# Kernel tuning notes

Hardware: AMD Instinct MI355X
Metric: run time of the kernel (lower is better)

Reference implementation:

```python
import jax, jax.numpy as jnp
import numpy as np

B, L = 64, 512
D_IN, D_POS = 256, 64
KS, VS, H = 64, 64, 8
OUT = 256
EPS = 1e-5
NEG = -1e30


def setup_inputs() -> dict:
    key = jax.random.key(0)
    ks = jax.random.split(key, 12)
    D = D_IN + D_POS
    s = 0.02
    return {
        "emb": jax.random.normal(ks[0], (B, L, D_IN), jnp.float32),
        "boxes": jax.random.normal(ks[1], (B, L, D_POS), jnp.float32),
        "lengths": jax.random.randint(ks[2], (B,), 1, L + 1, jnp.int32),
        "Wq": jax.random.normal(ks[3], (D, H * KS), jnp.float32) * s,
        "Wk": jax.random.normal(ks[4], (D, H * KS), jnp.float32) * s,
        "Wv": jax.random.normal(ks[5], (D, H * VS), jnp.float32) * s,
        "W1": jax.random.normal(ks[6], (H * VS, OUT), jnp.float32) * s,
        "b1": jnp.zeros((OUT,), jnp.float32),
        "W2": jax.random.normal(ks[7], (OUT, OUT), jnp.float32) * s,
        "b2": jnp.zeros((OUT,), jnp.float32),
        "g1": jnp.ones((OUT,), jnp.float32),
        "be1": jnp.zeros((OUT,), jnp.float32),
        "g2": jnp.ones((OUT,), jnp.float32),
        "be2": jnp.zeros((OUT,), jnp.float32),
    }


def masked_bn(x, m, cnt, gamma, beta):
    # BatchNorm1d (training stats) over valid tokens only; x: [B,L,C], m: [B,L,1]
    mean = jnp.sum(x * m, axis=(0, 1)) / cnt
    var = jnp.sum(((x - mean) ** 2) * m, axis=(0, 1)) / cnt
    return gamma * (x - mean) * jax.lax.rsqrt(var + EPS) + beta


def reference(emb, boxes, lengths, Wq, Wk, Wv, W1, b1, W2, b2, g1, be1, g2, be2):
    X = jnp.concatenate([emb, boxes], axis=-1)  # [B,L,D]
    valid = (jnp.arange(L)[None, :] < lengths[:, None])  # [B,L] bool
    m = valid[..., None].astype(X.dtype)  # [B,L,1]
    cnt = jnp.sum(m)

    D = X.shape[-1]
    Q = jnp.einsum('bld,dhk->bhlk', X, Wq.reshape(D, H, KS))
    K = jnp.einsum('bld,dhk->bhlk', X, Wk.reshape(D, H, KS))
    V = jnp.einsum('bld,dhv->bhlv', X, Wv.reshape(D, H, VS))

    scores = jnp.einsum('bhqk,bhmk->bhqm', Q, K) / jnp.sqrt(jnp.float32(KS))
    scores = jnp.where(valid[:, None, None, :], scores, NEG)  # mask keys
    A = jax.nn.softmax(scores, axis=-1)  # [B,H,L,L]
    Z = jnp.einsum('bhqm,bhmv->bhqv', A, V)  # [B,H,L,V]
    Z = jnp.transpose(Z, (0, 2, 1, 3)).reshape(B, L, H * VS)

    # agregate: Linear -> BN -> ReLU -> (dropout=identity, eval) -> Linear -> BN + skip -> ReLU
    Z1 = Z @ W1 + b1
    Z1 = jax.nn.relu(masked_bn(Z1, m, cnt, g1, be1)) * m
    Z2 = Z1 @ W2 + b2
    out = jax.nn.relu(masked_bn(Z2, m, cnt, g2, be2) + emb) * m
    return out  # padded [B,L,OUT]; invalid positions zeroed
```

## Files before the change

kernel.cpp:

```cpp
#include <hip/hip_runtime.h>
#include <hip/hip_bf16.h>
#include <cstdio>

#define B_    64
#define L_    512
#define DIN   256
#define DPOS  64
#define DD    320
#define HH    8
#define ROWS  (B_*L_)
#define NQKV  1536

typedef __attribute__((ext_vector_type(4))) float floatx4;
typedef __attribute__((ext_vector_type(8))) __bf16 bf16x8;
typedef __attribute__((ext_vector_type(4))) __bf16 bf16x4;

static __device__ __forceinline__ floatx4 mfma_bf16(bf16x8 a, bf16x8 b, floatx4 c) {
  return __builtin_amdgcn_mfma_f32_16x16x32_bf16(a, b, c, 0, 0, 0);
}

#define GLOAD_LDS(gp, lp) \
  __builtin_amdgcn_global_load_lds((const __attribute__((address_space(1))) void*)(gp), \
                                   (__attribute__((address_space(3))) void*)(lp), 16, 0, 0)

__global__ __launch_bounds__(256)
void prep_emb(const float* __restrict__ emb, __hip_bfloat16* __restrict__ X) {
  int idx = blockIdx.x * 256 + threadIdx.x;
  int row = idx >> 6, c4 = (idx & 63) * 4;
  const float4 v = *(const float4*)(emb + (size_t)idx * 4);
  bf16x4 o; o[0] = (__bf16)v.x; o[1] = (__bf16)v.y; o[2] = (__bf16)v.z; o[3] = (__bf16)v.w;
  *(bf16x4*)((__bf16*)X + (size_t)row * DD + c4) = o;
}

__global__ __launch_bounds__(256)
void prep_box(const float* __restrict__ boxes, __hip_bfloat16* __restrict__ X) {
  int idx = blockIdx.x * 256 + threadIdx.x;
  int row = idx >> 4, c4 = (idx & 15) * 4;
  const float4 v = *(const float4*)(boxes + (size_t)idx * 4);
  bf16x4 o; o[0] = (__bf16)v.x; o[1] = (__bf16)v.y; o[2] = (__bf16)v.z; o[3] = (__bf16)v.w;
  *(bf16x4*)((__bf16*)X + (size_t)row * DD + DIN + c4) = o;
}

__global__ __launch_bounds__(256)
void prep_w(const float* __restrict__ Wq, const float* __restrict__ Wk,
            const float* __restrict__ Wv, const float* __restrict__ W1,
            const float* __restrict__ W2,
            __hip_bfloat16* __restrict__ WqkvT, __hip_bfloat16* __restrict__ W1T,
            __hip_bfloat16* __restrict__ W2T) {
  int n = blockIdx.x, t = threadIdx.x;
  if (n < NQKV) {
    const float* W = (n < 512) ? Wq : (n < 1024) ? Wk : Wv;
    int nn = n & 511;
    for (int k = t; k < DD; k += 256)
      WqkvT[(size_t)n*DD + k] = __float2bfloat16(W[(size_t)k*512 + nn]);
  } else if (n < NQKV + 256) {
    int nn = n - NQKV;
    for (int k = t; k < 512; k += 256)
      W1T[(size_t)nn*512 + k] = __float2bfloat16(W1[(size_t)k*256 + nn]);
  } else {
    int nn = n - NQKV - 256;
    for (int k = t; k < 256; k += 256)
      W2T[(size_t)nn*256 + k] = __float2bfloat16(W2[(size_t)k*256 + nn]);
  }
}

template<int EPI>
__global__ __launch_bounds__(256, 4)
void gemm_bt(const __hip_bfloat16* __restrict__ A, const __hip_bfloat16* __restrict__ BT,
             int nbx, int M, int N, int K, int lda,
             float* __restrict__ outF, const float* __restrict__ bias,
             __hip_bfloat16* __restrict__ outQK, __hip_bfloat16* __restrict__ outVT,
             const int* __restrict__ lengths, float* __restrict__ pS,
             float* __restrict__ pS2) {
  __shared__ __align__(16) __bf16 sm[17408];
  int hw = blockIdx.x;
  int lidx = (hw & 7) * ((int)gridDim.x >> 3) + (hw >> 3);
  int bx = lidx % nbx, by = lidx / nbx;
  int t = threadIdx.x;
  int m0 = by * 128, n0 = bx * 128;
  int wave = t >> 6, lane = t & 63, lr = lane & 15, lg = lane >> 4;
  int wr = wave >> 1, wc = wave & 1;
  floatx4 acc[4][4];
#pragma unroll
  for (int i = 0; i < 4; ++i)
#pragma unroll
    for (int j = 0; j < 4; ++j)
#pragma unroll
      for (int q = 0; q < 4; ++q) acc[i][j][q] = 0.f;

  int srow = t >> 2, ssl = t & 3;
  int scb = ssl ^ ((srow >> 2) & 3);
  const __bf16* gA = (const __bf16*)A + (size_t)(m0 + srow) * lda + scb * 8;
  const __bf16* gB = (const __bf16*)BT + (size_t)(n0 + srow) * K + scb * 8;

  auto stage = [&](int k0, int buf) {
    __bf16* Ad = sm + buf * 4096;
    __bf16* Bd = sm + 8192 + buf * 4096;
    GLOAD_LDS(gA + k0, Ad + t * 8);
    GLOAD_LDS(gA + (size_t)64 * lda + k0, Ad + (256 + t) * 8);
    GLOAD_LDS(gB + k0, Bd + t * 8);
    GLOAD_LDS(gB + (size_t)64 * K + k0, Bd + (256 + t) * 8);
  };

  int fs = (lr >> 2) & 3;
  int aoff[4], boff[4];
#pragma unroll
  for (int i = 0; i < 4; ++i) {
    aoff[i] = (wr*64 + i*16 + lr) * 32 + ((lg ^ fs) * 8);
    boff[i] = (wc*64 + i*16 + lr) * 32 + ((lg ^ fs) * 8);
  }

  int NK = K >> 5;
  stage(0, 0);
  __syncthreads();
  for (int kt = 0; kt < NK; ++kt) {
    int cur = kt & 1;
    if (kt + 1 < NK) stage((kt + 1) << 5, cur ^ 1);
    const __bf16* As = sm + cur * 4096;
    const __bf16* Bs = sm + 8192 + cur * 4096;
    bf16x8 af[4], bfr[4];
#pragma unroll
    for (int i = 0; i < 4; ++i) af[i]  = *(const bf16x8*)(As + aoff[i]);
#pragma unroll
    for (int j = 0; j < 4; ++j) bfr[j] = *(const bf16x8*)(Bs + boff[j]);
    __builtin_amdgcn_s_setprio(1);
#pragma unroll
    for (int i = 0; i < 4; ++i)
#pragma unroll
      for (int j = 0; j < 4; ++j)
        acc[i][j] = mfma_bf16(af[i], bfr[j], acc[i][j]);
    __builtin_amdgcn_s_setprio(0);
    __syncthreads();
  }

  if (EPI == 1) {
    int lenb = lengths[m0 >> 9];
    int lbase = m0 & 511;
    float s1[4] = {0.f,0.f,0.f,0.f}, s2[4] = {0.f,0.f,0.f,0.f};
#pragma unroll
    for (int i = 0; i < 4; ++i)
#pragma unroll
      for (int j = 0; j < 4; ++j)
#pragma unroll
        for (int q = 0; q < 4; ++q) {
          int rrow = wr*64 + i*16 + lg*4 + q;
          int col = n0 + wc*64 + j*16 + lr;
          float v = acc[i][j][q] + bias[col];
          outF[(size_t)(m0 + rrow) * N + col] = v;
          if (lbase + rrow < lenb) { s1[j] += v; s2[j] += v*v; }
        }
#pragma unroll
    for (int j = 0; j < 4; ++j) {
      s1[j] += __shfl_xor(s1[j], 16); s1[j] += __shfl_xor(s1[j], 32);
      s2[j] += __shfl_xor(s2[j], 16); s2[j] += __shfl_xor(s2[j], 32);
    }
    float* fb = (float*)sm;
    if (lg == 0) {
#pragma unroll
      for (int j = 0; j < 4; ++j) {
        int cloc = wc*64 + j*16 + lr;
        fb[wr*128 + cloc] = s1[j];
        fb[256 + wr*128 + cloc] = s2[j];
      }
    }
    __syncthreads();
    if (t < 128) {
      pS [by*256 + bx*128 + t] = fb[t] + fb[128 + t];
      pS2[by*256 + bx*128 + t] = fb[256 + t] + fb[384 + t];
    }
  } else if (n0 < 1024) {
#pragma unroll
    for (int i = 0; i < 4; ++i)
#pragma unroll
      for (int j = 0; j < 4; ++j)
#pragma unroll
        for (int q = 0; q < 4; ++q) {
          int row = m0 + wr*64 + i*16 + lg*4 + q;
          int col = n0 + wc*64 + j*16 + lr;
          outQK[(size_t)row * 1024 + col] = __float2bfloat16(acc[i][j][q]);
        }
  } else {
    __bf16* Ct = sm;
#pragma unroll
    for (int i = 0; i < 4; ++i)
#pragma unroll
      for (int j = 0; j < 4; ++j) {
        int col = wc*64 + j*16 + lr;
        int row0 = wr*64 + i*16 + lg*4;
        bf16x4 pv;
#pragma unroll
        for (int q = 0; q < 4; ++q) pv[q] = (__bf16)acc[i][j][q];
        *(bf16x4*)(Ct + col*136 + row0) = pv;
      }
    __syncthreads();
    int b = m0 >> 9, l0 = m0 & 511, gcol0 = n0 - 1024;
#pragma unroll
    for (int it = 0; it < 8; ++it) {
      int g = it * 256 + t;
      int vv = g >> 4, rc = g & 15;
      bf16x8 val = *(const bf16x8*)(Ct + vv*136 + rc*8);
      int gc = gcol0 + vv, h = gc >> 6, vg = gc & 63;
      *(bf16x8*)((__bf16*)outVT + ((size_t)((b*HH + h)*64 + vg))*512 + l0 + rc*8) = val;
    }
  }
}

__global__ __launch_bounds__(512)
void attn(__hip_bfloat16* QK, const __hip_bfloat16* __restrict__ VT,
          const int* __restrict__ lengths) {
  int hw = blockIdx.x;
  int h = hw & 7, qt = (hw >> 3) & 3, b = hw >> 5;
  int len = lengths[b];
  if (qt * 128 >= len) return;
  __shared__ __align__(16) __hip_bfloat16 Ks[2][4096];
  __shared__ __align__(16) __hip_bfloat16 Vs[2][4096];
  __shared__ __align__(16) __hip_bfloat16 P[8][16][72];
  int t = threadIdx.x, wave = t >> 6, lane = t & 63, lr = lane & 15, lg = lane >> 4;
  int q0 = qt * 128 + wave * 16;
  const __hip_bfloat16* Qb = QK + (size_t)b*512*1024 + h*64;
  const __hip_bfloat16* Kb = QK + (size_t)b*512*1024 + 512 + h*64;
  const __hip_bfloat16* Vb = VT + (size_t)(b*HH + h)*64*512;

  bf16x8 qf0 = *(const bf16x8*)(Qb + (size_t)(q0 + lr)*1024 + lg*8);
  bf16x8 qf1 = *(const bf16x8*)(Qb + (size_t)(q0 + lr)*1024 + 32 + lg*8);
#pragma unroll
  for (int i = 0; i < 8; ++i) {
    qf0[i] = (__bf16)((float)qf0[i] * 0.125f);
    qf1[i] = (__bf16)((float)qf1[i] * 0.125f);
  }
  bf16x8 onesf;
#pragma unroll
  for (int i = 0; i < 8; ++i) onesf[i] = (__bf16)1.0f;

  int off0[4], off1[4];
#pragma unroll
  for (int r4 = 0; r4 < 4; ++r4) {
    int row = r4*16 + lr, sw = row & 7;
    off0[r4] = row*64 + ((lg ^ sw) * 8);
    off1[r4] = row*64 + (((lg + 4) ^ sw) * 8);
  }
  int srow = t >> 3, scb = t & 7;
  int scbd = scb ^ (srow & 7);
  const __hip_bfloat16* kgp = Kb + (size_t)srow*1024 + scbd*8;
  const __hip_bfloat16* vgp = Vb + (size_t)srow*512 + scbd*8;

  int nt = (len + 63) >> 6;

  auto stage = [&](int kt, int buf) {
    GLOAD_LDS(kgp + (size_t)kt*65536, &Ks[buf][t*8]);
    GLOAD_LDS(vgp + kt*64, &Vs[buf][t*8]);
  };

  floatx4 O[4];
  floatx4 Ol = {0.f, 0.f, 0.f, 0.f};
#pragma unroll
  for (int vb = 0; vb < 4; ++vb)
#pragma unroll
    for (int i = 0; i < 4; ++i) O[vb][i] = 0.f;

  stage(0, 0);
  __syncthreads();

  for (int kt = 0; kt < nt; ++kt) {
    int cur = kt & 1;
    if (kt + 1 < nt) stage(kt + 1, cur ^ 1);
    int kb0 = kt * 64;
    const __hip_bfloat16* Kc = Ks[cur];
    const __hip_bfloat16* Vc = Vs[cur];

    floatx4 S[4];
    __builtin_amdgcn_s_setprio(1);
#pragma unroll
    for (int kb = 0; kb < 4; ++kb) {
      bf16x8 kf0 = *(const bf16x8*)(Kc + off0[kb]);
      bf16x8 kf1 = *(const bf16x8*)(Kc + off1[kb]);
      floatx4 s = {0.f, 0.f, 0.f, 0.f};
      s = mfma_bf16(kf0, qf0, s);
      s = mfma_bf16(kf1, qf1, s);
      S[kb] = s;
    }
    __builtin_amdgcn_s_setprio(0);
#pragma unroll
    for (int kb = 0; kb < 4; ++kb)
#pragma unroll
      for (int i = 0; i < 4; ++i) S[kb][i] = __expf(S[kb][i]);
    if (kb0 + 64 > len) {
#pragma unroll
      for (int kb = 0; kb < 4; ++kb)
#pragma unroll
        for (int i = 0; i < 4; ++i)
          if (kb0 + kb*16 + lg*4 + i >= len) S[kb][i] = 0.f;
    }
#pragma unroll
    for (int kb = 0; kb < 4; ++kb) {
      bf16x4 pv;
#pragma unroll
      for (int i = 0; i < 4; ++i) pv[i] = (__bf16)S[kb][i];
      *(bf16x4*)(&P[wave][lr][kb*16 + lg*4]) = pv;
    }
    bf16x8 pf0 = *(const bf16x8*)(&P[wave][lr][lg*8]);
    bf16x8 pf1 = *(const bf16x8*)(&P[wave][lr][32 + lg*8]);
    __builtin_amdgcn_s_setprio(1);
#pragma unroll
    for (int vb = 0; vb < 4; ++vb) {
      bf16x8 vf0 = *(const bf16x8*)(Vc + off0[vb]);
      bf16x8 vf1 = *(const bf16x8*)(Vc + off1[vb]);
      O[vb] = mfma_bf16(pf0, vf0, O[vb]);
      O[vb] = mfma_bf16(pf1, vf1, O[vb]);
    }
    Ol = mfma_bf16(pf0, onesf, Ol);
    Ol = mfma_bf16(pf1, onesf, Ol);
    __builtin_amdgcn_s_setprio(0);
    __syncthreads();
  }

#pragma unroll
  for (int vb = 0; vb < 4; ++vb)
#pragma unroll
    for (int i = 0; i < 4; ++i) {
      int q = q0 + lg*4 + i;
      float z = O[vb][i] / Ol[i];
      QK[(size_t)(b*512 + q)*1024 + h*64 + vb*16 + lr] = __float2bfloat16(z);
    }
}

__global__ __launch_bounds__(256)
void stats_fin(const float* __restrict__ pS, const float* __restrict__ pS2,
               const int* __restrict__ lengths, const float* __restrict__ g,
               const float* __restrict__ be, float* __restrict__ aff) {
  int t = threadIdx.x;
  float cnt = 0.f;
  for (int i = 0; i < 64; ++i) cnt += (float)lengths[i];
  float s = 0.f, s2 = 0.f;
  for (int i = 0; i < 256; ++i) { s += pS[i*256 + t]; s2 += pS2[i*256 + t]; }
  float mean = s / cnt;
  float var = s2 / cnt - mean * mean;
  float a = g[t] * rsqrtf(var + 1e-5f);
  aff[t] = a;
  aff[256 + t] = be[t] - mean * a;
}

__global__ __launch_bounds__(256)
void apply1(const float* __restrict__ Zr, const int* __restrict__ lengths,
            const float* __restrict__ aff, __hip_bfloat16* __restrict__ Zn) {
  int idx = blockIdx.x * 256 + threadIdx.x;
  int row = idx >> 6, c4 = (idx & 63) * 4;
  int b = row >> 9, l = row & 511;
  bool ok = l < lengths[b];
  float4 v = *(const float4*)(Zr + (size_t)row*256 + c4);
  float4 a = *(const float4*)(aff + c4);
  float4 c = *(const float4*)(aff + 256 + c4);
  bf16x4 o;
  o[0] = (__bf16)(ok ? fmaxf(a.x*v.x + c.x, 0.f) : 0.f);
  o[1] = (__bf16)(ok ? fmaxf(a.y*v.y + c.y, 0.f) : 0.f);
  o[2] = (__bf16)(ok ? fmaxf(a.z*v.z + c.z, 0.f) : 0.f);
  o[3] = (__bf16)(ok ? fmaxf(a.w*v.w + c.w, 0.f) : 0.f);
  *(bf16x4*)((__bf16*)Zn + (size_t)row*256 + c4) = o;
}

__global__ __launch_bounds__(256)
void apply2(const float* __restrict__ Zr, const float* __restrict__ emb,
            const int* __restrict__ lengths, const float* __restrict__ aff,
            float* __restrict__ out) {
  int idx = blockIdx.x * 256 + threadIdx.x;
  int row = idx >> 6, c4 = (idx & 63) * 4;
  int b = row >> 9, l = row & 511;
  bool ok = l < lengths[b];
  size_t base = (size_t)row*256 + c4;
  float4 v = *(const float4*)(Zr + base);
  float4 e = *(const float4*)(emb + base);
  float4 a = *(const float4*)(aff + c4);
  float4 c = *(const float4*)(aff + 256 + c4);
  float4 o;
  o.x = ok ? fmaxf(a.x*v.x + c.x + e.x, 0.f) : 0.f;
  o.y = ok ? fmaxf(a.y*v.y + c.y + e.y, 0.f) : 0.f;
  o.z = ok ? fmaxf(a.z*v.z + c.z + e.z, 0.f) : 0.f;
  o.w = ok ? fmaxf(a.w*v.w + c.w + e.w, 0.f) : 0.f;
  *(float4*)(out + base) = o;
}

extern "C" void kernel_launch(void* const* d_in, const int* in_sizes, int n_in,
                              void* d_out, int out_size, void* d_ws, size_t ws_size,
                              hipStream_t stream) {
  const float* emb   = (const float*)d_in[0];
  const float* boxes = (const float*)d_in[1];
  const int*   dlen  = (const int*)d_in[2];
  const float* Wq    = (const float*)d_in[3];
  const float* Wk    = (const float*)d_in[4];
  const float* Wv    = (const float*)d_in[5];
  const float* W1    = (const float*)d_in[6];
  const float* b1    = (const float*)d_in[7];
  const float* W2    = (const float*)d_in[8];
  const float* b2    = (const float*)d_in[9];
  const float* g1    = (const float*)d_in[10];
  const float* be1   = (const float*)d_in[11];
  const float* g2    = (const float*)d_in[12];
  const float* be2   = (const float*)d_in[13];
  float* out = (float*)d_out;

  const size_t oWqkvT = 0;
  const size_t oW1T   = 983040;
  const size_t oW2T   = 1245184;
  const size_t oAff1  = 1376256;
  const size_t oAff2  = 1378304;
  const size_t oPS    = 1380352;
  const size_t oPS2   = 1642496;
  const size_t oXbf   = 1904640;
  const size_t oQK    = 22876160;
  const size_t oVT    = 89985024;
  const size_t NEED   = 123539456;
  if (ws_size < NEED) { fprintf(stderr, "ws too small: %zu < %zu\n", ws_size, NEED); return; }

  char* w = (char*)d_ws;
  __hip_bfloat16* WqkvT = (__hip_bfloat16*)(w + oWqkvT);
  __hip_bfloat16* W1T   = (__hip_bfloat16*)(w + oW1T);
  __hip_bfloat16* W2T   = (__hip_bfloat16*)(w + oW2T);
  float* aff1 = (float*)(w + oAff1);
  float* aff2 = (float*)(w + oAff2);
  float* pS   = (float*)(w + oPS);
  float* pS2  = (float*)(w + oPS2);
  __hip_bfloat16* Xbf = (__hip_bfloat16*)(w + oXbf);
  __hip_bfloat16* Z1n = (__hip_bfloat16*)(w + oXbf);
  __hip_bfloat16* QK  = (__hip_bfloat16*)(w + oQK);
  float* Z2raw = (float*)(w + oQK);
  __hip_bfloat16* VT  = (__hip_bfloat16*)(w + oVT);
  float* Z1raw = (float*)(w + oVT);

  prep_emb<<<ROWS/4, 256, 0, stream>>>(emb, Xbf);
  prep_box<<<ROWS/16, 256, 0, stream>>>(boxes, Xbf);
  prep_w<<<2048, 256, 0, stream>>>(Wq, Wk, Wv, W1, W2, WqkvT, W1T, W2T);
  gemm_bt<0><<<12*256, 256, 0, stream>>>(
      Xbf, WqkvT, 12, ROWS, NQKV, DD, DD, nullptr, nullptr, QK, VT,
      nullptr, nullptr, nullptr);
  attn<<<2048, 512, 0, stream>>>(QK, VT, dlen);
  gemm_bt<1><<<2*256, 256, 0, stream>>>(
      QK, W1T, 2, ROWS, 256, 512, 1024, Z1raw, b1, nullptr, nullptr,
      dlen, pS, pS2);
  stats_fin<<<1, 256, 0, stream>>>(pS, pS2, dlen, g1, be1, aff1);
  apply1<<<ROWS/4, 256, 0, stream>>>(Z1raw, dlen, aff1, Z1n);
  gemm_bt<1><<<2*256, 256, 0, stream>>>(
      Z1n, W2T, 2, ROWS, 256, 256, 256, Z2raw, b2, nullptr, nullptr,
      dlen, pS, pS2);
  stats_fin<<<1, 256, 0, stream>>>(pS, pS2, dlen, g2, be2, aff2);
  apply2<<<ROWS/4, 256, 0, stream>>>(Z2raw, emb, dlen, aff2, out);
}
```

Measured before the change: 182.0 us.

## Skip padded GEMM tiles, deepen K-tile to 64, tile weight transpose

GEMM blocks whose 128-row tile lies entirely beyond the sequence length now exit early, writing zero partial statistics for BN tiles, so no matmul work is spent on padding rows. The GEMM K-step grows from 32 to 64 with a wider XOR swizzle and doubled LDS, halving barrier count per tile, and the occupancy hint is dropped. Weight transposition moves from 2048 strided-load blocks to 32 blocks using an LDS tile for coalesced access. Skipped QKV tiles leave Q/K/V unwritten for padded rows, which is safe only if attention and later stages ignore those rows.

```diff
diff --git a/kernel.cpp b/kernel.cpp
--- a/kernel.cpp
+++ b/kernel.cpp
@@ -47,37 +47,60 @@
             const float* __restrict__ W2,
             __hip_bfloat16* __restrict__ WqkvT, __hip_bfloat16* __restrict__ W1T,
             __hip_bfloat16* __restrict__ W2T) {
-  int n = blockIdx.x, t = threadIdx.x;
-  if (n < NQKV) {
-    const float* W = (n < 512) ? Wq : (n < 1024) ? Wk : Wv;
-    int nn = n & 511;
-    for (int k = t; k < DD; k += 256)
-      WqkvT[(size_t)n*DD + k] = __float2bfloat16(W[(size_t)k*512 + nn]);
-  } else if (n < NQKV + 256) {
-    int nn = n - NQKV;
-    for (int k = t; k < 512; k += 256)
-      W1T[(size_t)nn*512 + k] = __float2bfloat16(W1[(size_t)k*256 + nn]);
+  __shared__ float tile[64][65];
+  int blk = blockIdx.x, t = threadIdx.x;
+  const float* src; __hip_bfloat16* dst; int n0, KD, ldsrc, lddst;
+  if (blk < 24) {
+    int m = blk >> 3;
+    src = (m == 0) ? Wq : (m == 1) ? Wk : Wv;
+    dst = WqkvT + (size_t)m * 512 * DD;
+    n0 = (blk & 7) * 64; KD = DD; ldsrc = 512; lddst = DD;
+  } else if (blk < 28) {
+    src = W1; dst = W1T; n0 = (blk - 24) * 64; KD = 512; ldsrc = 256; lddst = 512;
   } else {
-    int nn = n - NQKV - 256;
-    for (int k = t; k < 256; k += 256)
-      W2T[(size_t)nn*256 + k] = __float2bfloat16(W2[(size_t)k*256 + nn]);
+    src = W2; dst = W2T; n0 = (blk - 28) * 64; KD = 256; ldsrc = 256; lddst = 256;
+  }
+  for (int k0 = 0; k0 < KD; k0 += 64) {
+#pragma unroll
+    for (int i = 0; i < 16; ++i) {
+      int e = i * 256 + t, kr = e >> 6, nc = e & 63;
+      tile[kr][nc] = src[(size_t)(k0 + kr) * ldsrc + n0 + nc];
+    }
+    __syncthreads();
+#pragma unroll
+    for (int i = 0; i < 4; ++i) {
+      int ww = i * 256 + t, nr = ww >> 4, kc = (ww & 15) * 4;
+      bf16x4 o;
+      o[0] = (__bf16)tile[kc][nr];   o[1] = (__bf16)tile[kc+1][nr];
+      o[2] = (__bf16)tile[kc+2][nr]; o[3] = (__bf16)tile[kc+3][nr];
+      *(bf16x4*)(dst + (size_t)(n0 + nr) * lddst + k0 + kc) = o;
+    }
+    __syncthreads();
   }
 }
 
 template<int EPI>
-__global__ __launch_bounds__(256, 4)
+__global__ __launch_bounds__(256)
 void gemm_bt(const __hip_bfloat16* __restrict__ A, const __hip_bfloat16* __restrict__ BT,
-             int nbx, int M, int N, int K, int lda,
+             int nbx, int N, int K, int lda,
              float* __restrict__ outF, const float* __restrict__ bias,
              __hip_bfloat16* __restrict__ outQK, __hip_bfloat16* __restrict__ outVT,
              const int* __restrict__ lengths, float* __restrict__ pS,
              float* __restrict__ pS2) {
-  __shared__ __align__(16) __bf16 sm[17408];
+  __shared__ __align__(16) __bf16 sm[32768];
   int hw = blockIdx.x;
   int lidx = (hw & 7) * ((int)gridDim.x >> 3) + (hw >> 3);
   int bx = lidx % nbx, by = lidx / nbx;
   int t = threadIdx.x;
   int m0 = by * 128, n0 = bx * 128;
+  int lenb = lengths[m0 >> 9];
+  if ((m0 & 511) >= lenb) {
+    if (EPI == 1 && t < 128) {
+      pS [by*256 + bx*128 + t] = 0.f;
+      pS2[by*256 + bx*128 + t] = 0.f;
+    }
+    return;
+  }
   int wave = t >> 6, lane = t & 63, lr = lane & 15, lg = lane >> 4;
   int wr = wave >> 1, wc = wave & 1;
   floatx4 acc[4][4];
@@ -88,53 +111,60 @@
 #pragma unroll
       for (int q = 0; q < 4; ++q) acc[i][j][q] = 0.f;
 
-  int srow = t >> 2, ssl = t & 3;
-  int scb = ssl ^ ((srow >> 2) & 3);
+  int srow = t >> 3;
+  int scb = (t & 7) ^ (srow & 7);
   const __bf16* gA = (const __bf16*)A + (size_t)(m0 + srow) * lda + scb * 8;
   const __bf16* gB = (const __bf16*)BT + (size_t)(n0 + srow) * K + scb * 8;
 
   auto stage = [&](int k0, int buf) {
-    __bf16* Ad = sm + buf * 4096;
-    __bf16* Bd = sm + 8192 + buf * 4096;
-    GLOAD_LDS(gA + k0, Ad + t * 8);
-    GLOAD_LDS(gA + (size_t)64 * lda + k0, Ad + (256 + t) * 8);
-    GLOAD_LDS(gB + k0, Bd + t * 8);
-    GLOAD_LDS(gB + (size_t)64 * K + k0, Bd + (256 + t) * 8);
+    __bf16* Ad = sm + buf * 8192;
+    __bf16* Bd = sm + 16384 + buf * 8192;
+#pragma unroll
+    for (int r = 0; r < 4; ++r) {
+      GLOAD_LDS(gA + (size_t)(r*32) * lda + k0, Ad + (r*256 + t) * 8);
+      GLOAD_LDS(gB + (size_t)(r*32) * K   + k0, Bd + (r*256 + t) * 8);
+    }
   };
 
-  int fs = (lr >> 2) & 3;
-  int aoff[4], boff[4];
+  int aoff[4][2], boff[4][2];
 #pragma unroll
   for (int i = 0; i < 4; ++i) {
-    aoff[i] = (wr*64 + i*16 + lr) * 32 + ((lg ^ fs) * 8);
-    boff[i] = (wc*64 + i*16 + lr) * 32 + ((lg ^ fs) * 8);
-  }
-
-  int NK = K >> 5;
+#pragma unroll
+    for (int ks = 0; ks < 2; ++ks) {
+      int ra = wr*64 + i*16 + lr;
+      int rb = wc*64 + i*16 + lr;
+      aoff[i][ks] = ra*64 + (((ks*4 + lg) ^ (ra & 7)) * 8);
+      boff[i][ks] = rb*64 + (((ks*4 + lg) ^ (rb & 7)) * 8);
+    }
+  }
+
+  int NK = K >> 6;
   stage(0, 0);
   __syncthreads();
   for (int kt = 0; kt < NK; ++kt) {
     int cur = kt & 1;
-    if (kt + 1 < NK) stage((kt + 1) << 5, cur ^ 1);
-    const __bf16* As = sm + cur * 4096;
-    const __bf16* Bs = sm + 8192 + cur * 4096;
-    bf16x8 af[4], bfr[4];
-#pragma unroll
-    for (int i = 0; i < 4; ++i) af[i]  = *(const bf16x8*)(As + aoff[i]);
-#pragma unroll
-    for (int j = 0; j < 4; ++j) bfr[j] = *(const bf16x8*)(Bs + boff[j]);
-    __builtin_amdgcn_s_setprio(1);
-#pragma unroll
-    for (int i = 0; i < 4; ++i)
-#pragma unroll
-      for (int j = 0; j < 4; ++j)
-        acc[i][j] = mfma_bf16(af[i], bfr[j], acc[i][j]);
-    __builtin_amdgcn_s_setprio(0);
+    if (kt + 1 < NK) stage((kt + 1) << 6, cur ^ 1);
+    const __bf16* As = sm + cur * 8192;
+    const __bf16* Bs = sm + 16384 + cur * 8192;
+#pragma unroll
+    for (int ks = 0; ks < 2; ++ks) {
+      bf16x8 af[4], bfr[4];
+#pragma unroll
+      for (int i = 0; i < 4; ++i) af[i]  = *(const bf16x8*)(As + aoff[i][ks]);
+#pragma unroll
+      for (int j = 0; j < 4; ++j) bfr[j] = *(const bf16x8*)(Bs + boff[j][ks]);
+      __builtin_amdgcn_s_setprio(1);
+#pragma unroll
+      for (int i = 0; i < 4; ++i)
+#pragma unroll
+        for (int j = 0; j < 4; ++j)
+          acc[i][j] = mfma_bf16(af[i], bfr[j], acc[i][j]);
+      __builtin_amdgcn_s_setprio(0);
+    }
     __syncthreads();
   }
 
   if (EPI == 1) {
-    int lenb = lengths[m0 >> 9];
     int lbase = m0 & 511;
     float s1[4] = {0.f,0.f,0.f,0.f}, s2[4] = {0.f,0.f,0.f,0.f};
 #pragma unroll
@@ -428,18 +458,18 @@
 
   prep_emb<<<ROWS/4, 256, 0, stream>>>(emb, Xbf);
   prep_box<<<ROWS/16, 256, 0, stream>>>(boxes, Xbf);
-  prep_w<<<2048, 256, 0, stream>>>(Wq, Wk, Wv, W1, W2, WqkvT, W1T, W2T);
+  prep_w<<<32, 256, 0, stream>>>(Wq, Wk, Wv, W1, W2, WqkvT, W1T, W2T);
   gemm_bt<0><<<12*256, 256, 0, stream>>>(
-      Xbf, WqkvT, 12, ROWS, NQKV, DD, DD, nullptr, nullptr, QK, VT,
-      nullptr, nullptr, nullptr);
+      Xbf, WqkvT, 12, NQKV, DD, DD, nullptr, nullptr, QK, VT,
+      dlen, nullptr, nullptr);
   attn<<<2048, 512, 0, stream>>>(QK, VT, dlen);
   gemm_bt<1><<<2*256, 256, 0, stream>>>(
-      QK, W1T, 2, ROWS, 256, 512, 1024, Z1raw, b1, nullptr, nullptr,
+      QK, W1T, 2, 256, 512, 1024, Z1raw, b1, nullptr, nullptr,
       dlen, pS, pS2);
   stats_fin<<<1, 256, 0, stream>>>(pS, pS2, dlen, g1, be1, aff1);
   apply1<<<ROWS/4, 256, 0, stream>>>(Z1raw, dlen, aff1, Z1n);
   gemm_bt<1><<<2*256, 256, 0, stream>>>(
-      Z1n, W2T, 2, ROWS, 256, 256, 256, Z2raw, b2, nullptr, nullptr,
+      Z1n, W2T, 2, 256, 256, 256, Z2raw, b2, nullptr, nullptr,
       dlen, pS, pS2);
   stats_fin<<<1, 256, 0, stream>>>(pS, pS2, dlen, g2, be2, aff2);
   apply2<<<ROWS/4, 256, 0, stream>>>(Z2raw, emb, dlen, aff2, out);
```

After: 191.5 us. +5.2%, slower.
